# Performance work log

Measured on AMD Instinct MI355X. Metric: run time of the kernel, lower is better.

## Reference

```python
import jax, jax.numpy as jnp
import numpy as np

D = 2048; H = 16; KV = 4; HD = D // H  # head_dim=128
EPS = 1e-6; THETA = 10000.0


def _rmsnorm(x, w):
    # x: [..., HD]
    var = jnp.mean(x * x, axis=-1, keepdims=True)
    return x * jax.lax.rsqrt(var + EPS) * w


def _rope(x, cos, sin):
    # x: [B, L, nH, HD]; cos/sin: [L, HD//2]; interleaved-pair rotation
    xe = x[..., 0::2]
    xo = x[..., 1::2]
    c = cos[None, :, None, :]
    s = sin[None, :, None, :]
    re = xe * c - xo * s
    ro = xe * s + xo * c
    return jnp.stack([re, ro], axis=-1).reshape(x.shape)


def setup_inputs() -> dict:
    key = jax.random.key(0)
    ks = jax.random.split(key, 8)
    B, L = 2, 2048
    x = jax.random.normal(ks[0], (B, L, D), dtype=jnp.float32)
    wq = jax.random.normal(ks[1], (D, D), dtype=jnp.float32) * 0.02
    wk = jax.random.normal(ks[2], (KV * HD, D), dtype=jnp.float32) * 0.02
    wv = jax.random.normal(ks[3], (KV * HD, D), dtype=jnp.float32) * 0.02
    wo = jax.random.normal(ks[4], (D, D), dtype=jnp.float32) * 0.02
    q_norm_w = jnp.ones((HD,), dtype=jnp.float32)
    k_norm_w = jnp.ones((HD,), dtype=jnp.float32)
    return {"x": x, "wq": wq, "wk": wk, "wv": wv, "wo": wo,
            "q_norm_w": q_norm_w, "k_norm_w": k_norm_w}


def reference(x, wq, wk, wv, wo, q_norm_w, k_norm_w):
    B, L, _ = x.shape
    G = H // KV  # GQA group size (repeat factor)

    q = (x @ wq.T).reshape(B, L, H, HD)
    k = (x @ wk.T).reshape(B, L, KV, HD)
    v = (x @ wv.T).reshape(B, L, KV, HD)

    q = _rmsnorm(q, q_norm_w)
    k = _rmsnorm(k, k_norm_w)

    # RoPE (positions 0..L-1, prompt path)
    inv_freq = 1.0 / (THETA ** (jnp.arange(0, HD, 2, dtype=jnp.float32) / HD))
    ang = jnp.arange(L, dtype=jnp.float32)[:, None] * inv_freq[None, :]  # [L, HD/2]
    cos, sin = jnp.cos(ang), jnp.sin(ang)
    q = _rope(q, cos, sin)
    k = _rope(k, cos, sin)

    # GQA: q head h attends kv head h // G (== repeat_interleave of k,v)
    qg = q.reshape(B, L, KV, G, HD)
    scale = 1.0 / jnp.sqrt(jnp.float32(HD))
    scores = jnp.einsum('bqkgd,bskd->bkgqs', qg, k) * scale  # [B,KV,G,L,L]

    causal = jnp.tril(jnp.ones((L, L), dtype=bool))
    scores = jnp.where(causal, scores, jnp.finfo(scores.dtype).min)
    p = jax.nn.softmax(scores, axis=-1)

    o = jnp.einsum('bkgqs,bskd->bqkgd', p, v).reshape(B, L, D)
    return o @ wo.T
```

## Files before the change

kernel.cpp:

```cpp
#include <hip/hip_runtime.h>
#include <hip/hip_bf16.h>
#include <stdint.h>
#include <stddef.h>

#define D_DIM 2048
#define H_HEADS 16
#define KV_HEADS 4
#define HEAD_DIM 128
#define SEQ_L 2048
#define BATCH 2
#define NTOK 4096
#define NQK 2560

typedef __attribute__((ext_vector_type(4))) float f32x4;
typedef __attribute__((ext_vector_type(16))) float f32x16;
typedef __attribute__((ext_vector_type(8))) short bf16x8;

__device__ __forceinline__ unsigned short f2bf(float f) {
  __hip_bfloat16 h = __float2bfloat16(f);
  return *reinterpret_cast<unsigned short*>(&h);
}
__device__ __forceinline__ unsigned pack2(float lo, float hi) {
  return (unsigned)f2bf(lo) | ((unsigned)f2bf(hi) << 16);
}
__device__ __forceinline__ float bf2f(unsigned short s) {
  return __uint_as_float(((unsigned int)s) << 16);
}

__device__ __forceinline__ void async_copy16(const void* g, void* l) {
  __builtin_amdgcn_global_load_lds(
      (__attribute__((address_space(1))) void*)(g),
      (__attribute__((address_space(3))) void*)(l),
      16, 0, 0);
}

__device__ __forceinline__ void cast_seg(const float* __restrict__ src,
                                         unsigned short* __restrict__ dst,
                                         int n4, int gid, int stride) {
  for (int i = gid; i < n4; i += stride) {
    float4 v = *reinterpret_cast<const float4*>(src + i * 4);
    uint2 o;
    o.x = pack2(v.x, v.y);
    o.y = pack2(v.z, v.w);
    *reinterpret_cast<uint2*>(dst + i * 4) = o;
  }
}

__global__ __launch_bounds__(256) void fused_cast_kernel(
    const float* __restrict__ s0, const float* __restrict__ s1,
    const float* __restrict__ s2, const float* __restrict__ s3,
    const float* __restrict__ s4,
    unsigned short* __restrict__ d0, unsigned short* __restrict__ d1,
    unsigned short* __restrict__ d2, unsigned short* __restrict__ d3,
    unsigned short* __restrict__ d4) {
  int gid = blockIdx.x * blockDim.x + threadIdx.x;
  int stride = gridDim.x * blockDim.x;
  cast_seg(s0, d0, (NTOK * D_DIM) / 4, gid, stride);
  cast_seg(s1, d1, (D_DIM * D_DIM) / 4, gid, stride);
  cast_seg(s2, d2, (512 * D_DIM) / 4, gid, stride);
  cast_seg(s3, d3, (512 * D_DIM) / 4, gid, stride);
  cast_seg(s4, d4, (D_DIM * D_DIM) / 4, gid, stride);
}

__global__ __launch_bounds__(256) void rope_table_kernel(float* __restrict__ cosT,
                                                         float* __restrict__ sinT) {
  int i = blockIdx.x * blockDim.x + threadIdx.x;
  if (i >= SEQ_L * 64) return;
  int p = i & 63;
  float l = (float)(i >> 6);
  float inv = powf(10000.0f, -(float)p / 64.0f);
  float ang = l * inv;
  cosT[i] = cosf(ang);
  sinT[i] = sinf(ang);
}

__device__ __forceinline__ void store_out(unsigned short* p, float v) { *p = f2bf(v); }
__device__ __forceinline__ void store_out(float* p, float v) { *p = v; }

template <typename OutT>
__global__ __launch_bounds__(256) void gemm_bt_kernel(const unsigned short* __restrict__ A,
                                                      const unsigned short* __restrict__ B,
                                                      OutT* __restrict__ C,
                                                      int M, int N, int K) {
  __shared__ unsigned short Alds[128 * 32];
  __shared__ unsigned short Blds[128 * 32];
  const int tid = threadIdx.x;
  const int wave = tid >> 6;
  const int lane = tid & 63;
  const int l15 = lane & 15;
  const int l4 = lane >> 4;

  const int nwg = gridDim.x * gridDim.y;
  const int orig = blockIdx.y * gridDim.x + blockIdx.x;
  const int cpx = nwg >> 3;
  const int swz = (orig & 7) * cpx + (orig >> 3);
  const int m0 = (swz % gridDim.x) * 128;
  const int n0 = (swz / gridDim.x) * 128;

  const int wm = (wave >> 1) * 64;
  const int wn = (wave & 1) * 64;

  f32x4 acc[4][4] = {};

  const int soff0 = wave * 1024 + lane * 16;

  for (int kt = 0; kt < K; kt += 32) {
#pragma unroll
    for (int inst = 0; inst < 2; ++inst) {
      int off = soff0 + inst * 4096;
      int row = off >> 6;
      int colb = off & 63;
      const char* ga = (const char*)(A + (size_t)(m0 + row) * K + kt) + colb;
      async_copy16(ga, (char*)Alds + off);
      const char* gb = (const char*)(B + (size_t)(n0 + row) * K + kt) + colb;
      async_copy16(gb, (char*)Blds + off);
    }
    __syncthreads();
    bf16x8 af[4], bfr[4];
#pragma unroll
    for (int i = 0; i < 4; ++i)
      af[i] = *reinterpret_cast<const bf16x8*>(Alds + (wm + i * 16 + l15) * 32 + l4 * 8);
#pragma unroll
    for (int j = 0; j < 4; ++j)
      bfr[j] = *reinterpret_cast<const bf16x8*>(Blds + (wn + j * 16 + l15) * 32 + l4 * 8);
#pragma unroll
    for (int i = 0; i < 4; ++i)
#pragma unroll
      for (int j = 0; j < 4; ++j)
        acc[i][j] = __builtin_amdgcn_mfma_f32_16x16x32_bf16(af[i], bfr[j], acc[i][j], 0, 0, 0);
    __syncthreads();
  }

#pragma unroll
  for (int i = 0; i < 4; ++i)
#pragma unroll
    for (int j = 0; j < 4; ++j) {
      int col = n0 + wn + j * 16 + l15;
#pragma unroll
      for (int r = 0; r < 4; ++r) {
        int row = m0 + wm + i * 16 + l4 * 4 + r;
        store_out(C + (size_t)row * N + col, acc[i][j][r]);
      }
    }
}

__global__ __launch_bounds__(256) void norm_rope_kernel(unsigned short* __restrict__ qk,
                                                        const float* __restrict__ qw,
                                                        const float* __restrict__ kw,
                                                        const float* __restrict__ cosT,
                                                        const float* __restrict__ sinT) {
  int wid = (blockIdx.x * blockDim.x + threadIdx.x) >> 6;
  int lane = threadIdx.x & 63;
  unsigned short* rowp;
  const float* w;
  int m;
  float sc;
  if (wid < NTOK * H_HEADS) {
    m = wid >> 4;
    int hh = wid & 15;
    rowp = qk + (size_t)m * NQK + hh * HEAD_DIM;
    w = qw;
    sc = 0.08838834764831845f;
  } else {
    int r2 = wid - NTOK * H_HEADS;
    m = r2 >> 2;
    int kvh = r2 & 3;
    rowp = qk + (size_t)m * NQK + D_DIM + kvh * HEAD_DIM;
    w = kw;
    sc = 1.0f;
  }
  int l = m & (SEQ_L - 1);
  unsigned int pair = *reinterpret_cast<const unsigned int*>(rowp + lane * 2);
  float e = bf2f((unsigned short)(pair & 0xffffu));
  float o = bf2f((unsigned short)(pair >> 16));
  float ss = e * e + o * o;
#pragma unroll
  for (int off = 1; off < 64; off <<= 1) ss += __shfl_xor(ss, off);
  float rsn = rsqrtf(ss * (1.0f / 128.0f) + 1e-6f) * sc;
  float we = w[lane * 2], wo_ = w[lane * 2 + 1];
  float c = cosT[l * 64 + lane], s = sinT[l * 64 + lane];
  float xe = e * rsn * we, xo = o * rsn * wo_;
  float re = xe * c - xo * s;
  float ro = xe * s + xo * c;
  *reinterpret_cast<unsigned int*>(rowp + lane * 2) = pack2(re, ro);
}

__global__ __launch_bounds__(128) void attn_kernel(const unsigned short* __restrict__ qk,
                                                   const unsigned short* __restrict__ vt,
                                                   unsigned short* __restrict__ obuf) {
  __shared__ unsigned short Kl[2][64 * 128];
  __shared__ unsigned short Vl[2][128 * 64];
  __shared__ float invl[64];

  const int tid = threadIdx.x;
  const int w = tid >> 6, lane = tid & 63;
  const int l31 = lane & 31, hi = lane >> 5;
  const int job = blockIdx.x;
  const int bh = blockIdx.y;
  const int b = bh >> 4, h = bh & 15, kvh = h >> 2;

  const unsigned short* Kg = qk + (size_t)(b * SEQ_L) * NQK + D_DIM + kvh * HEAD_DIM;
  const unsigned short* Vg = vt + (size_t)(kvh * HEAD_DIM) * NTOK + b * SEQ_L;

  auto stage = [&](int bb, int kt) {
#pragma unroll
    for (int i = 0; i < 8; ++i) {
      int o = (i * 128 + tid) * 16;
      {
        int row = o >> 8;
        int scb = (o & 255) ^ ((row & 7) << 4);
        const char* src = (const char*)(Kg + (size_t)(kt * 64 + row) * NQK) + scb;
        async_copy16(src, (char*)(&Kl[bb][0]) + o);
      }
      {
        int d = o >> 7;
        int skb = (o & 127) ^ ((d & 7) << 4);
        const char* src = (const char*)(Vg + (size_t)d * NTOK + kt * 64) + skb;
        async_copy16(src, (char*)(&Vl[bb][0]) + o);
      }
    }
  };

#pragma unroll 1
  for (int jj = 0; jj < 2; ++jj) {
    const int jt = jj ? (31 - job) : job;
    const int q0 = jt * 64;
    const int ntiles = jt + 1;

    const unsigned short* Qg =
        qk + (size_t)(b * SEQ_L + q0 + w * 32 + l31) * NQK + h * HEAD_DIM;
    bf16x8 qf[8];
#pragma unroll
    for (int kk = 0; kk < 8; ++kk)
      qf[kk] = *reinterpret_cast<const bf16x8*>(Qg + kk * 16 + hi * 8);

    f32x16 accO[4] = {};
    float m_run = -1e30f, l_run = 0.0f;

    const int qmin_w = q0 + w * 32;
    const int qg = qmin_w + l31;

    stage(0, 0);
    asm volatile("s_waitcnt vmcnt(0)" ::: "memory");
    __syncthreads();

    int buf = 0;
    for (int kt = 0; kt < ntiles; ++kt) {
      if (kt + 1 < ntiles) stage(buf ^ 1, kt + 1);

      {
        f32x16 st[2] = {};
        __builtin_amdgcn_s_setprio(1);
#pragma unroll
        for (int stile = 0; stile < 2; ++stile) {
#pragma unroll
          for (int kk = 0; kk < 8; ++kk) {
            int row = stile * 32 + l31;
            int off = (row << 8) + (((kk << 5) + (hi << 4)) ^ ((l31 & 7) << 4));
            bf16x8 kf = *reinterpret_cast<const bf16x8*>((const char*)(&Kl[buf][0]) + off);
            st[stile] = __builtin_amdgcn_mfma_f32_32x32x16_bf16(kf, qf[kk], st[stile], 0, 0, 0);
          }
        }
        __builtin_amdgcn_s_setprio(0);

        const bool need_mask = (kt * 64 + 63 > qmin_w);
        float tmax = -1e30f;
#pragma unroll
        for (int stile = 0; stile < 2; ++stile)
#pragma unroll
          for (int r = 0; r < 16; ++r) {
            float s = st[stile][r];
            if (need_mask) {
              int key = kt * 64 + stile * 32 + (r & 3) + ((r >> 2) << 3) + (hi << 2);
              if (key > qg) s = -1e30f;
            }
            st[stile][r] = s;
            tmax = fmaxf(tmax, s);
          }
        tmax = fmaxf(tmax, __shfl_xor(tmax, 32));

        if (!__all(tmax - m_run <= 8.0f)) {
          float mnew = fmaxf(m_run, tmax);
          float corr = __expf(m_run - mnew);
          m_run = mnew;
          l_run *= corr;
          float corrq[16];
#pragma unroll
          for (int r = 0; r < 16; ++r) {
            int qi = (r & 3) + ((r >> 2) << 3) + (hi << 2);
            corrq[r] = __shfl(corr, qi);
          }
#pragma unroll
          for (int dt = 0; dt < 4; ++dt)
#pragma unroll
            for (int r = 0; r < 16; ++r) accO[dt][r] *= corrq[r];
        }

        float rsum = 0.0f;
#pragma unroll
        for (int stile = 0; stile < 2; ++stile)
#pragma unroll
          for (int r = 0; r < 16; ++r) {
            float pe = __expf(st[stile][r] - m_run);
            st[stile][r] = pe;
            rsum += pe;
          }
        rsum += __shfl_xor(rsum, 32);
        l_run += rsum;

        bf16x8 pa[2][2];
#pragma unroll
        for (int stile = 0; stile < 2; ++stile)
#pragma unroll
          for (int kc = 0; kc < 2; ++kc) {
            int rb = kc * 8;
            unsigned x0 = pack2(st[stile][rb + 0], st[stile][rb + 1]);
            unsigned y0 = pack2(st[stile][rb + 4], st[stile][rb + 5]);
            unsigned x1 = pack2(st[stile][rb + 2], st[stile][rb + 3]);
            unsigned y1 = pack2(st[stile][rb + 6], st[stile][rb + 7]);
            unsigned x0s = (unsigned)__shfl_xor((int)x0, 32);
            unsigned y0s = (unsigned)__shfl_xor((int)y0, 32);
            unsigned x1s = (unsigned)__shfl_xor((int)x1, 32);
            unsigned y1s = (unsigned)__shfl_xor((int)y1, 32);
            unsigned w0 = hi ? y0s : x0;
            unsigned w2 = hi ? y0 : x0s;
            unsigned w1 = hi ? y1s : x1;
            unsigned w3 = hi ? y1 : x1s;
            union { bf16x8 v; unsigned u[4]; } uu;
            uu.u[0] = w0; uu.u[1] = w1; uu.u[2] = w2; uu.u[3] = w3;
            pa[stile][kc] = uu.v;
          }

        __builtin_amdgcn_s_setprio(1);
#pragma unroll
        for (int dt = 0; dt < 4; ++dt) {
          int drow = dt * 32 + l31;
#pragma unroll
          for (int stile = 0; stile < 2; ++stile)
#pragma unroll
            for (int kc = 0; kc < 2; ++kc) {
              int off = (drow << 7) + (((stile << 6) + (kc << 5) + (hi << 4)) ^ ((l31 & 7) << 4));
              bf16x8 vf = *reinterpret_cast<const bf16x8*>((const char*)(&Vl[buf][0]) + off);
              accO[dt] = __builtin_amdgcn_mfma_f32_32x32x16_bf16(pa[stile][kc], vf, accO[dt], 0, 0, 0);
            }
        }
        __builtin_amdgcn_s_setprio(0);
      }

      asm volatile("s_waitcnt vmcnt(0)" ::: "memory");
      __syncthreads();
      buf ^= 1;
    }

    if (hi == 0) invl[w * 32 + l31] = 1.0f / l_run;
    __syncthreads();
#pragma unroll
    for (int dt = 0; dt < 4; ++dt)
#pragma unroll
      for (int r = 0; r < 16; ++r) {
        int qrow = (r & 3) + ((r >> 2) << 3) + (hi << 2);
        float val = accO[dt][r] * invl[w * 32 + qrow];
        int tok = b * SEQ_L + q0 + w * 32 + qrow;
        obuf[(size_t)tok * D_DIM + h * HEAD_DIM + dt * 32 + l31] = f2bf(val);
      }
    __syncthreads();
  }
}

extern "C" void kernel_launch(void* const* d_in, const int* in_sizes, int n_in,
                              void* d_out, int out_size, void* d_ws, size_t ws_size,
                              hipStream_t stream) {
  const float* x   = (const float*)d_in[0];
  const float* wq  = (const float*)d_in[1];
  const float* wk  = (const float*)d_in[2];
  const float* wv  = (const float*)d_in[3];
  const float* wo  = (const float*)d_in[4];
  const float* qnw = (const float*)d_in[5];
  const float* knw = (const float*)d_in[6];
  float* out = (float*)d_out;

  char* ws = (char*)d_ws;
  unsigned short* Xb   = (unsigned short*)(ws);
  unsigned short* Wqkb = (unsigned short*)(ws + 16777216);
  unsigned short* Wvb  = (unsigned short*)(ws + 27262976);
  unsigned short* Wob  = (unsigned short*)(ws + 29360128);
  unsigned short* QKb  = (unsigned short*)(ws + 37748736);
  unsigned short* VTb  = (unsigned short*)(ws + 58720256);
  unsigned short* Obuf = (unsigned short*)(ws + 62914560);
  float* cosT = (float*)(ws + 79691776);
  float* sinT = (float*)(ws + 80216064);

  fused_cast_kernel<<<1024, 256, 0, stream>>>(
      x, wq, wk, wv, wo,
      Xb, Wqkb, Wqkb + (size_t)D_DIM * D_DIM, Wvb, Wob);
  rope_table_kernel<<<512, 256, 0, stream>>>(cosT, sinT);

  dim3 g1(NTOK / 128, NQK / 128);
  gemm_bt_kernel<unsigned short><<<g1, 256, 0, stream>>>(Xb, Wqkb, QKb, NTOK, NQK, D_DIM);

  dim3 gv(512 / 128, NTOK / 128);
  gemm_bt_kernel<unsigned short><<<gv, 256, 0, stream>>>(Wvb, Xb, VTb, 512, NTOK, D_DIM);

  norm_rope_kernel<<<(NTOK * (H_HEADS + KV_HEADS)) / 4, 256, 0, stream>>>(QKb, qnw, knw, cosT, sinT);

  attn_kernel<<<dim3(16, BATCH * H_HEADS), 128, 0, stream>>>(QKb, VTb, Obuf);

  dim3 g2(NTOK / 128, D_DIM / 128);
  gemm_bt_kernel<float><<<g2, 256, 0, stream>>>(Obuf, Wob, out, NTOK, D_DIM, D_DIM);
}
```

Before: 294.4 us.

## Fuse V projection into QK GEMM and retile attention to 128-query blocks

Merges the separate V-projection GEMM into the QK GEMM by concatenating the weights, so one launch covers all QKV columns. Blocks whose tile lands in the V region write transposed bf16 output straight into the VT buffer. The attention kernel moves from 2 waves handling two paired 64-query tiles to 4 waves on one 128-query tile, processed heaviest-first, with K/V staging shared across 4 waves. This removes one launch and improves K/V reuse per tile. The cost is less load balance, since the diagonal pairing is gone, and a skip branch for waves with no work on the final tiles.

```diff
diff --git a/kernel.cpp b/kernel.cpp
--- a/kernel.cpp
+++ b/kernel.cpp
@@ -11,6 +11,7 @@
 #define BATCH 2
 #define NTOK 4096
 #define NQK 2560
+#define NQKV 3072
 
 typedef __attribute__((ext_vector_type(4))) float f32x4;
 typedef __attribute__((ext_vector_type(16))) float f32x16;
@@ -77,10 +78,11 @@
 __device__ __forceinline__ void store_out(unsigned short* p, float v) { *p = f2bf(v); }
 __device__ __forceinline__ void store_out(float* p, float v) { *p = v; }
 
-template <typename OutT>
+template <typename OutT, bool VSPLIT>
 __global__ __launch_bounds__(256) void gemm_bt_kernel(const unsigned short* __restrict__ A,
                                                       const unsigned short* __restrict__ B,
                                                       OutT* __restrict__ C,
+                                                      unsigned short* __restrict__ vt,
                                                       int M, int N, int K) {
   __shared__ unsigned short Alds[128 * 32];
   __shared__ unsigned short Blds[128 * 32];
@@ -131,6 +133,24 @@
     __syncthreads();
   }
 
+  if (VSPLIT && n0 >= NQK) {
+#pragma unroll
+    for (int i = 0; i < 4; ++i)
+#pragma unroll
+      for (int j = 0; j < 4; ++j) {
+        int vrow = n0 + wn + j * 16 + l15 - NQK;
+        int tok0 = m0 + wm + i * 16 + l4 * 4;
+        ushort4 pk;
+        pk.x = f2bf(acc[i][j][0]);
+        pk.y = f2bf(acc[i][j][1]);
+        pk.z = f2bf(acc[i][j][2]);
+        pk.w = f2bf(acc[i][j][3]);
+        *reinterpret_cast<ushort4*>(vt + (size_t)vrow * NTOK + tok0) = pk;
+      }
+    return;
+  }
+
+  const int cstride = VSPLIT ? NQK : N;
 #pragma unroll
   for (int i = 0; i < 4; ++i)
 #pragma unroll
@@ -139,7 +159,7 @@
 #pragma unroll
       for (int r = 0; r < 4; ++r) {
         int row = m0 + wm + i * 16 + l4 * 4 + r;
-        store_out(C + (size_t)row * N + col, acc[i][j][r]);
+        store_out(C + (size_t)row * cstride + col, acc[i][j][r]);
       }
     }
 }
@@ -185,27 +205,42 @@
   *reinterpret_cast<unsigned int*>(rowp + lane * 2) = pack2(re, ro);
 }
 
-__global__ __launch_bounds__(128) void attn_kernel(const unsigned short* __restrict__ qk,
-                                                   const unsigned short* __restrict__ vt,
-                                                   unsigned short* __restrict__ obuf) {
+__global__ __launch_bounds__(256, 2) void attn_kernel(const unsigned short* __restrict__ qk,
+                                                      const unsigned short* __restrict__ vt,
+                                                      unsigned short* __restrict__ obuf) {
   __shared__ unsigned short Kl[2][64 * 128];
   __shared__ unsigned short Vl[2][128 * 64];
-  __shared__ float invl[64];
+  __shared__ float invl[128];
 
   const int tid = threadIdx.x;
   const int w = tid >> 6, lane = tid & 63;
   const int l31 = lane & 31, hi = lane >> 5;
-  const int job = blockIdx.x;
+  const int qt = gridDim.x - 1 - blockIdx.x;
+  const int q0 = qt * 128;
   const int bh = blockIdx.y;
   const int b = bh >> 4, h = bh & 15, kvh = h >> 2;
 
+  const unsigned short* Qg = qk + (size_t)(b * SEQ_L + q0 + w * 32 + l31) * NQK + h * HEAD_DIM;
   const unsigned short* Kg = qk + (size_t)(b * SEQ_L) * NQK + D_DIM + kvh * HEAD_DIM;
   const unsigned short* Vg = vt + (size_t)(kvh * HEAD_DIM) * NTOK + b * SEQ_L;
 
+  bf16x8 qf[8];
+#pragma unroll
+  for (int kk = 0; kk < 8; ++kk)
+    qf[kk] = *reinterpret_cast<const bf16x8*>(Qg + kk * 16 + hi * 8);
+
+  f32x16 accO[4] = {};
+  float m_run = -1e30f, l_run = 0.0f;
+
+  const int qmin_w = q0 + w * 32;
+  const int qmax_w = qmin_w + 31;
+  const int qg = qmin_w + l31;
+  const int ntiles = (q0 + 128) >> 6;
+
   auto stage = [&](int bb, int kt) {
 #pragma unroll
-    for (int i = 0; i < 8; ++i) {
-      int o = (i * 128 + tid) * 16;
+    for (int i = 0; i < 4; ++i) {
+      int o = (i * 256 + tid) * 16;
       {
         int row = o >> 8;
         int scb = (o & 255) ^ ((row & 7) << 4);
@@ -221,150 +256,129 @@
     }
   };
 
-#pragma unroll 1
-  for (int jj = 0; jj < 2; ++jj) {
-    const int jt = jj ? (31 - job) : job;
-    const int q0 = jt * 64;
-    const int ntiles = jt + 1;
-
-    const unsigned short* Qg =
-        qk + (size_t)(b * SEQ_L + q0 + w * 32 + l31) * NQK + h * HEAD_DIM;
-    bf16x8 qf[8];
-#pragma unroll
-    for (int kk = 0; kk < 8; ++kk)
-      qf[kk] = *reinterpret_cast<const bf16x8*>(Qg + kk * 16 + hi * 8);
-
-    f32x16 accO[4] = {};
-    float m_run = -1e30f, l_run = 0.0f;
-
-    const int qmin_w = q0 + w * 32;
-    const int qg = qmin_w + l31;
-
-    stage(0, 0);
+  stage(0, 0);
+  asm volatile("s_waitcnt vmcnt(0)" ::: "memory");
+  __syncthreads();
+
+  int buf = 0;
+  for (int kt = 0; kt < ntiles; ++kt) {
+    if (kt + 1 < ntiles) stage(buf ^ 1, kt + 1);
+
+    if (kt * 64 <= qmax_w) {
+      f32x16 st[2] = {};
+      __builtin_amdgcn_s_setprio(1);
+#pragma unroll
+      for (int stile = 0; stile < 2; ++stile) {
+#pragma unroll
+        for (int kk = 0; kk < 8; ++kk) {
+          int row = stile * 32 + l31;
+          int off = (row << 8) + (((kk << 5) + (hi << 4)) ^ ((l31 & 7) << 4));
+          bf16x8 kf = *reinterpret_cast<const bf16x8*>((const char*)(&Kl[buf][0]) + off);
+          st[stile] = __builtin_amdgcn_mfma_f32_32x32x16_bf16(kf, qf[kk], st[stile], 0, 0, 0);
+        }
+      }
+      __builtin_amdgcn_s_setprio(0);
+
+      const bool need_mask = (kt * 64 + 63 > qmin_w);
+      float tmax = -1e30f;
+#pragma unroll
+      for (int stile = 0; stile < 2; ++stile)
+#pragma unroll
+        for (int r = 0; r < 16; ++r) {
+          float s = st[stile][r];
+          if (need_mask) {
+            int key = kt * 64 + stile * 32 + (r & 3) + ((r >> 2) << 3) + (hi << 2);
+            if (key > qg) s = -1e30f;
+          }
+          st[stile][r] = s;
+          tmax = fmaxf(tmax, s);
+        }
+      tmax = fmaxf(tmax, __shfl_xor(tmax, 32));
+
+      if (!__all(tmax - m_run <= 8.0f)) {
+        float mnew = fmaxf(m_run, tmax);
+        float corr = __expf(m_run - mnew);
+        m_run = mnew;
+        l_run *= corr;
+        float corrq[16];
+#pragma unroll
+        for (int r = 0; r < 16; ++r) {
+          int qi = (r & 3) + ((r >> 2) << 3) + (hi << 2);
+          corrq[r] = __shfl(corr, qi);
+        }
+#pragma unroll
+        for (int dt = 0; dt < 4; ++dt)
+#pragma unroll
+          for (int r = 0; r < 16; ++r) accO[dt][r] *= corrq[r];
+      }
+
+      float rsum = 0.0f;
+#pragma unroll
+      for (int stile = 0; stile < 2; ++stile)
+#pragma unroll
+        for (int r = 0; r < 16; ++r) {
+          float pe = __expf(st[stile][r] - m_run);
+          st[stile][r] = pe;
+          rsum += pe;
+        }
+      rsum += __shfl_xor(rsum, 32);
+      l_run += rsum;
+
+      bf16x8 pa[2][2];
+#pragma unroll
+      for (int stile = 0; stile < 2; ++stile)
+#pragma unroll
+        for (int kc = 0; kc < 2; ++kc) {
+          int rb = kc * 8;
+          unsigned x0 = pack2(st[stile][rb + 0], st[stile][rb + 1]);
+          unsigned y0 = pack2(st[stile][rb + 4], st[stile][rb + 5]);
+          unsigned x1 = pack2(st[stile][rb + 2], st[stile][rb + 3]);
+          unsigned y1 = pack2(st[stile][rb + 6], st[stile][rb + 7]);
+          unsigned x0s = (unsigned)__shfl_xor((int)x0, 32);
+          unsigned y0s = (unsigned)__shfl_xor((int)y0, 32);
+          unsigned x1s = (unsigned)__shfl_xor((int)x1, 32);
+          unsigned y1s = (unsigned)__shfl_xor((int)y1, 32);
+          unsigned w0 = hi ? y0s : x0;
+          unsigned w2 = hi ? y0 : x0s;
+          unsigned w1 = hi ? y1s : x1;
+          unsigned w3 = hi ? y1 : x1s;
+          union { bf16x8 v; unsigned u[4]; } uu;
+          uu.u[0] = w0; uu.u[1] = w1; uu.u[2] = w2; uu.u[3] = w3;
+          pa[stile][kc] = uu.v;
+        }
+
+      __builtin_amdgcn_s_setprio(1);
+#pragma unroll
+      for (int dt = 0; dt < 4; ++dt) {
+        int drow = dt * 32 + l31;
+#pragma unroll
+        for (int stile = 0; stile < 2; ++stile)
+#pragma unroll
+          for (int kc = 0; kc < 2; ++kc) {
+            int off = (drow << 7) + (((stile << 6) + (kc << 5) + (hi << 4)) ^ ((l31 & 7) << 4));
+            bf16x8 vf = *reinterpret_cast<const bf16x8*>((const char*)(&Vl[buf][0]) + off);
+            accO[dt] = __builtin_amdgcn_mfma_f32_32x32x16_bf16(pa[stile][kc], vf, accO[dt], 0, 0, 0);
+          }
+      }
+      __builtin_amdgcn_s_setprio(0);
+    }
+
     asm volatile("s_waitcnt vmcnt(0)" ::: "memory");
     __syncthreads();
-
-    int buf = 0;
-    for (int kt = 0; kt < ntiles; ++kt) {
-      if (kt + 1 < ntiles) stage(buf ^ 1, kt + 1);
-
-      {
-        f32x16 st[2] = {};
-        __builtin_amdgcn_s_setprio(1);
-#pragma unroll
-        for (int stile = 0; stile < 2; ++stile) {
-#pragma unroll
-          for (int kk = 0; kk < 8; ++kk) {
-            int row = stile * 32 + l31;
-            int off = (row << 8) + (((kk << 5) + (hi << 4)) ^ ((l31 & 7) << 4));
-            bf16x8 kf = *reinterpret_cast<const bf16x8*>((const char*)(&Kl[buf][0]) + off);
-            st[stile] = __builtin_amdgcn_mfma_f32_32x32x16_bf16(kf, qf[kk], st[stile], 0, 0, 0);
-          }
-        }
-        __builtin_amdgcn_s_setprio(0);
-
-        const bool need_mask = (kt * 64 + 63 > qmin_w);
-        float tmax = -1e30f;
-#pragma unroll
-        for (int stile = 0; stile < 2; ++stile)
-#pragma unroll
-          for (int r = 0; r < 16; ++r) {
-            float s = st[stile][r];
-            if (need_mask) {
-              int key = kt * 64 + stile * 32 + (r & 3) + ((r >> 2) << 3) + (hi << 2);
-              if (key > qg) s = -1e30f;
-            }
-            st[stile][r] = s;
-            tmax = fmaxf(tmax, s);
-          }
-        tmax = fmaxf(tmax, __shfl_xor(tmax, 32));
-
-        if (!__all(tmax - m_run <= 8.0f)) {
-          float mnew = fmaxf(m_run, tmax);
-          float corr = __expf(m_run - mnew);
-          m_run = mnew;
-          l_run *= corr;
-          float corrq[16];
-#pragma unroll
-          for (int r = 0; r < 16; ++r) {
-            int qi = (r & 3) + ((r >> 2) << 3) + (hi << 2);
-            corrq[r] = __shfl(corr, qi);
-          }
-#pragma unroll
-          for (int dt = 0; dt < 4; ++dt)
-#pragma unroll
-            for (int r = 0; r < 16; ++r) accO[dt][r] *= corrq[r];
-        }
-
-        float rsum = 0.0f;
-#pragma unroll
-        for (int stile = 0; stile < 2; ++stile)
-#pragma unroll
-          for (int r = 0; r < 16; ++r) {
-            float pe = __expf(st[stile][r] - m_run);
-            st[stile][r] = pe;
-            rsum += pe;
-          }
-        rsum += __shfl_xor(rsum, 32);
-        l_run += rsum;
-
-        bf16x8 pa[2][2];
-#pragma unroll
-        for (int stile = 0; stile < 2; ++stile)
-#pragma unroll
-          for (int kc = 0; kc < 2; ++kc) {
-            int rb = kc * 8;
-            unsigned x0 = pack2(st[stile][rb + 0], st[stile][rb + 1]);
-            unsigned y0 = pack2(st[stile][rb + 4], st[stile][rb + 5]);
-            unsigned x1 = pack2(st[stile][rb + 2], st[stile][rb + 3]);
-            unsigned y1 = pack2(st[stile][rb + 6], st[stile][rb + 7]);
-            unsigned x0s = (unsigned)__shfl_xor((int)x0, 32);
-            unsigned y0s = (unsigned)__shfl_xor((int)y0, 32);
-            unsigned x1s = (unsigned)__shfl_xor((int)x1, 32);
-            unsigned y1s = (unsigned)__shfl_xor((int)y1, 32);
-            unsigned w0 = hi ? y0s : x0;
-            unsigned w2 = hi ? y0 : x0s;
-            unsigned w1 = hi ? y1s : x1;
-            unsigned w3 = hi ? y1 : x1s;
-            union { bf16x8 v; unsigned u[4]; } uu;
-            uu.u[0] = w0; uu.u[1] = w1; uu.u[2] = w2; uu.u[3] = w3;
-            pa[stile][kc] = uu.v;
-          }
-
-        __builtin_amdgcn_s_setprio(1);
-#pragma unroll
-        for (int dt = 0; dt < 4; ++dt) {
-          int drow = dt * 32 + l31;
-#pragma unroll
-          for (int stile = 0; stile < 2; ++stile)
-#pragma unroll
-            for (int kc = 0; kc < 2; ++kc) {
-              int off = (drow << 7) + (((stile << 6) + (kc << 5) + (hi << 4)) ^ ((l31 & 7) << 4));
-              bf16x8 vf = *reinterpret_cast<const bf16x8*>((const char*)(&Vl[buf][0]) + off);
-              accO[dt] = __builtin_amdgcn_mfma_f32_32x32x16_bf16(pa[stile][kc], vf, accO[dt], 0, 0, 0);
-            }
-        }
-        __builtin_amdgcn_s_setprio(0);
-      }
-
-      asm volatile("s_waitcnt vmcnt(0)" ::: "memory");
-      __syncthreads();
-      buf ^= 1;
+    buf ^= 1;
+  }
+
+  if (hi == 0) invl[w * 32 + l31] = 1.0f / l_run;
+  __syncthreads();
+#pragma unroll
+  for (int dt = 0; dt < 4; ++dt)
+#pragma unroll
+    for (int r = 0; r < 16; ++r) {
+      int qrow = (r & 3) + ((r >> 2) << 3) + (hi << 2);
+      float val = accO[dt][r] * invl[w * 32 + qrow];
+      int tok = b * SEQ_L + q0 + w * 32 + qrow;
+      obuf[(size_t)tok * D_DIM + h * HEAD_DIM + dt * 32 + l31] = f2bf(val);
     }
-
-    if (hi == 0) invl[w * 32 + l31] = 1.0f / l_run;
-    __syncthreads();
-#pragma unroll
-    for (int dt = 0; dt < 4; ++dt)
-#pragma unroll
-      for (int r = 0; r < 16; ++r) {
-        int qrow = (r & 3) + ((r >> 2) << 3) + (hi << 2);
-        float val = accO[dt][r] * invl[w * 32 + qrow];
-        int tok = b * SEQ_L + q0 + w * 32 + qrow;
-        obuf[(size_t)tok * D_DIM + h * HEAD_DIM + dt * 32 + l31] = f2bf(val);
-      }
-    __syncthreads();
-  }
 }
 
 extern "C" void kernel_launch(void* const* d_in, const int* in_sizes, int n_in,
@@ -380,31 +394,31 @@
   float* out = (float*)d_out;
 
   char* ws = (char*)d_ws;
-  unsigned short* Xb   = (unsigned short*)(ws);
-  unsigned short* Wqkb = (unsigned short*)(ws + 16777216);
-  unsigned short* Wvb  = (unsigned short*)(ws + 27262976);
-  unsigned short* Wob  = (unsigned short*)(ws + 29360128);
-  unsigned short* QKb  = (unsigned short*)(ws + 37748736);
-  unsigned short* VTb  = (unsigned short*)(ws + 58720256);
-  unsigned short* Obuf = (unsigned short*)(ws + 62914560);
+  unsigned short* Xb    = (unsigned short*)(ws);
+  unsigned short* Wqkvb = (unsigned short*)(ws + 16777216);
+  unsigned short* Wob   = (unsigned short*)(ws + 29360128);
+  unsigned short* QKb   = (unsigned short*)(ws + 37748736);
+  unsigned short* VTb   = (unsigned short*)(ws + 58720256);
+  unsigned short* Obuf  = (unsigned short*)(ws + 62914560);
   float* cosT = (float*)(ws + 79691776);
   float* sinT = (float*)(ws + 80216064);
 
   fused_cast_kernel<<<1024, 256, 0, stream>>>(
       x, wq, wk, wv, wo,
-      Xb, Wqkb, Wqkb + (size_t)D_DIM * D_DIM, Wvb, Wob);
+      Xb, Wqkvb,
+      Wqkvb + (size_t)D_DIM * D_DIM,
+      Wqkvb + (size_t)NQK * D_DIM,
+      Wob);
   rope_table_kernel<<<512, 256, 0, stream>>>(cosT, sinT);
 
-  dim3 g1(NTOK / 128, NQK / 128);
-  gemm_bt_kernel<unsigned short><<<g1, 256, 0, stream>>>(Xb, Wqkb, QKb, NTOK, NQK, D_DIM);
-
-  dim3 gv(512 / 128, NTOK / 128);
-  gemm_bt_kernel<unsigned short><<<gv, 256, 0, stream>>>(Wvb, Xb, VTb, 512, NTOK, D_DIM);
+  dim3 g1(NTOK / 128, NQKV / 128);
+  gemm_bt_kernel<unsigned short, true><<<g1, 256, 0, stream>>>(
+      Xb, Wqkvb, QKb, VTb, NTOK, NQKV, D_DIM);
 
   norm_rope_kernel<<<(NTOK * (H_HEADS + KV_HEADS)) / 4, 256, 0, stream>>>(QKb, qnw, knw, cosT, sinT);
 
-  attn_kernel<<<dim3(16, BATCH * H_HEADS), 128, 0, stream>>>(QKb, VTb, Obuf);
+  attn_kernel<<<dim3(SEQ_L / 128, BATCH * H_HEADS), 256, 0, stream>>>(QKb, VTb, Obuf);
 
   dim3 g2(NTOK / 128, D_DIM / 128);
-  gemm_bt_kernel<float><<<g2, 256, 0, stream>>>(Obuf, Wob, out, NTOK, D_DIM, D_DIM);
-}
+  gemm_bt_kernel<float, false><<<g2, 256, 0, stream>>>(Obuf, Wob, out, nullptr, NTOK, D_DIM, D_DIM);
+}
```

New measurement: 260.3 us. 1.13x faster.
